# Kernel optimization log

Hardware: AMD Instinct MI355X
Metric: run time of the kernel (lower is better)

Reference implementation:

```python
import jax, jax.numpy as jnp
import numpy as np

N_ITER = 50


def sparsemax_bisect(X, n_iter=N_ITER):
    # entmax-style bisection for sparsemax (alpha=2): p = clip(X - tau, 0), sum(p) = 1
    d = X.shape[-1]
    max_val = jnp.max(X, axis=-1, keepdims=True)          # [N, 1]
    tau_lo = max_val - 1.0                                # f(tau_lo) >= 0
    tau_hi = max_val - 1.0 / d                            # f(tau_hi) <= 0
    f_lo = jnp.sum(jnp.clip(X - tau_lo, 0.0), axis=-1, keepdims=True) - 1.0
    dm0 = tau_hi - tau_lo

    def body(_, carry):
        tau_lo, dm, _tau_m = carry
        dm = dm * 0.5
        tau_m = tau_lo + dm
        f_m = jnp.sum(jnp.clip(X - tau_m, 0.0), axis=-1, keepdims=True) - 1.0
        tau_lo = jnp.where(f_m * f_lo >= 0, tau_m, tau_lo)
        return (tau_lo, dm, tau_m)

    _, _, tau_m = jax.lax.fori_loop(0, n_iter, body, (tau_lo, dm0, tau_lo))
    # p from the final midpoint, exactly as in entmax's sparsemax_bisect
    return jnp.clip(X - tau_m, 0.0)


def setup_inputs() -> dict:
    key = jax.random.key(0)
    X = jax.random.normal(key, (4096, 32000), dtype=jnp.float32)
    return {"X": X}


def reference(X):
    p_star = sparsemax_bisect(X, N_ITER)
    p_star = p_star / jnp.sum(p_star, axis=-1, keepdims=True)
    # log(0) -> -inf, matching torch.log on exact zeros
    sup = p_star > 0
    return jnp.where(sup, jnp.log(jnp.where(sup, p_star, 1.0)), -jnp.inf)
```

## Files before the change

kernel.cpp:

```cpp
#include <hip/hip_runtime.h>
#include <math.h>


typedef float f32x4 __attribute__((ext_vector_type(4)));

#define ROWS 4096
#define COLS 32000
#define NV4  (COLS / 4)
#define TPB  256
#define WPB  (TPB / 64)
#define U    4
#define SEG  512
#define CAP  (SEG * WPB)
#define REGC 4
#define SENT (-1e38f)
#define QMIN (1e-37f)

__global__ __launch_bounds__(TPB, 6)
void logsparsemax_v8_kernel(const float* __restrict__ X,
                            float* __restrict__ Y) {
    __shared__ float s_cand[CAP];
    __shared__ int   s_cidx[CAP];
    __shared__ float s_wmax[WPB];
    __shared__ int   s_wcnt[WPB];
    __shared__ float s_res[2];

    const int tid  = threadIdx.x;
    const int lane = tid & 63;
    const int wid  = tid >> 6;
    const int row  = blockIdx.x;
    const float* __restrict__ Xr = X + (size_t)row * COLS;
    const f32x4* __restrict__ X4 = (const f32x4*)Xr;
    float* __restrict__ Yr = Y + (size_t)row * COLS;
    f32x4* __restrict__ Y4 = (f32x4*)Yr;

    const f32x4 sent4 = {SENT, SENT, SENT, SENT};
    const int sbase = wid * SEG;

    float wmax = -INFINITY;
    float thr  = -INFINITY;
    int   cnt  = 0;

    int i = tid;
    f32x4 cur[U];
    #pragma unroll
    for (int u = 0; u < U; ++u) cur[u] = X4[i + u * TPB];

    while (i + (U - 1) * TPB < NV4) {
        const int inext = i + U * TPB;
        const bool hn = (inext + (U - 1) * TPB < NV4);
        f32x4 nxt[U];
        if (hn) {
            #pragma unroll
            for (int u = 0; u < U; ++u) nxt[u] = X4[inext + u * TPB];
        }
        #pragma unroll
        for (int u = 0; u < U; ++u) Y4[i + u * TPB] = sent4;

        float mall = -INFINITY;
        #pragma unroll
        for (int u = 0; u < U; ++u)
            mall = fmaxf(mall, fmaxf(fmaxf(cur[u].x, cur[u].y), fmaxf(cur[u].z, cur[u].w)));

        if (__ballot(mall > thr) != 0ull) {
            float t = mall;
            #pragma unroll
            for (int off = 32; off > 0; off >>= 1)
                t = fmaxf(t, __shfl_xor(t, off, 64));
            wmax = fmaxf(wmax, t);
            thr  = wmax - 1.0f;
            #pragma unroll
            for (int u = 0; u < U; ++u) {
                float vv[4] = {cur[u].x, cur[u].y, cur[u].z, cur[u].w};
                #pragma unroll
                for (int c = 0; c < 4; ++c) {
                    bool p = vv[c] > thr;
                    unsigned long long m = __ballot(p);
                    if (p) {
                        int pos = cnt + __popcll(m & ((1ull << lane) - 1ull));
                        if (pos < SEG) {
                            s_cand[sbase + pos] = vv[c];
                            s_cidx[sbase + pos] = 4 * (i + u * TPB) + c;
                        }
                    }
                    cnt += __popcll(m);
                }
            }
        }

        #pragma unroll
        for (int u = 0; u < U; ++u) cur[u] = nxt[u];
        i = inext;
    }
    for (; i < NV4; i += TPB) {
        f32x4 a = X4[i];
        Y4[i] = sent4;
        float mall = fmaxf(fmaxf(a.x, a.y), fmaxf(a.z, a.w));
        if (__ballot(mall > thr) != 0ull) {
            float t = mall;
            #pragma unroll
            for (int off = 32; off > 0; off >>= 1)
                t = fmaxf(t, __shfl_xor(t, off, 64));
            wmax = fmaxf(wmax, t);
            thr  = wmax - 1.0f;
            float vv[4] = {a.x, a.y, a.z, a.w};
            #pragma unroll
            for (int c = 0; c < 4; ++c) {
                bool p = vv[c] > thr;
                unsigned long long m = __ballot(p);
                if (p) {
                    int pos = cnt + __popcll(m & ((1ull << lane) - 1ull));
                    if (pos < SEG) {
                        s_cand[sbase + pos] = vv[c];
                        s_cidx[sbase + pos] = 4 * i + c;
                    }
                }
                cnt += __popcll(m);
            }
        }
    }

    if (lane == 0) { s_wmax[wid] = wmax; s_wcnt[wid] = cnt; }
    __syncthreads();

    const float bmax = fmaxf(fmaxf(s_wmax[0], s_wmax[1]), fmaxf(s_wmax[2], s_wmax[3]));
    const float tau_lo0 = bmax - 1.0f;
    const float tau_hi0 = bmax - (float)(1.0 / (double)COLS);
    const bool  fast = (s_wcnt[0] <= SEG) && (s_wcnt[1] <= SEG) &&
                       (s_wcnt[2] <= SEG) && (s_wcnt[3] <= SEG);

    if (wid == 0) {
        int nf = 0;
        if (fast) {
            for (int w = 0; w < WPB; ++w) {
                const int cw = s_wcnt[w];
                for (int j0 = 0; j0 < cw; j0 += 64) {
                    const int j = j0 + lane;
                    const bool in = (j < cw);
                    float v  = in ? s_cand[w * SEG + j] : 0.0f;
                    int   ix = in ? s_cidx[w * SEG + j] : 0;
                    bool  k  = in && (v > tau_lo0);
                    unsigned long long m = __ballot(k);
                    if (k) {
                        int pos = nf + __popcll(m & ((1ull << lane) - 1ull));
                        s_cand[pos] = v;
                        s_cidx[pos] = ix;
                    }
                    nf += __popcll(m);
                }
            }
        }

        float creg[REGC];
        #pragma unroll
        for (int k = 0; k < REGC; ++k) {
            int j = lane + 64 * k;
            creg[k] = (fast && j < nf) ? s_cand[j] : SENT;
        }

        auto fsum = [&](float tau) -> float {
            float acc = 0.0f;
            if (fast) {
                #pragma unroll
                for (int k = 0; k < REGC; ++k) acc += fmaxf(creg[k] - tau, 0.0f);
                for (int j = 64 * REGC + lane; j < nf; j += 64)
                    acc += fmaxf(s_cand[j] - tau, 0.0f);
            } else {
                for (int j = lane; j < COLS; j += 64)
                    acc += fmaxf(Xr[j] - tau, 0.0f);
            }
            #pragma unroll
            for (int off = 32; off > 0; off >>= 1)
                acc += __shfl_xor(acc, off, 64);
            return acc;
        };

        float tau_lo = tau_lo0;
        float dm     = tau_hi0 - tau_lo0;
        float tau_m  = tau_lo;
        const float f_lo = fsum(tau_lo) - 1.0f;
        for (int it = 0; it < 50; ++it) {
            dm *= 0.5f;
            float tcur = tau_lo + dm;
            tau_m = tcur;
            if (tcur == tau_lo) break;
            float f_m = fsum(tcur) - 1.0f;
            if (f_m * f_lo >= 0.0f) tau_lo = tcur;
        }
        const float ssum = fsum(tau_m);
        if (lane == 0) { s_res[0] = tau_m; s_res[1] = ssum; }

        if (fast) {
            const float lsm = logf(fmaxf(ssum, QMIN));
            for (int j = lane; j < nf; j += 64) {
                float r = s_cand[j] - tau_m;
                if (r > 0.0f)
                    Yr[s_cidx[j]] = logf(fmaxf(r, QMIN)) - lsm;
            }
        }
    }
    __syncthreads();

    if (!fast) {
        const float tau = s_res[0];
        const float lsm = logf(fmaxf(s_res[1], QMIN));
        for (int v4i = tid; v4i < NV4; v4i += TPB) {
            f32x4 v = X4[v4i];
            f32x4 o;
            float r;
            r = v.x - tau; o.x = (r > 0.0f) ? logf(fmaxf(r, QMIN)) - lsm : SENT;
            r = v.y - tau; o.y = (r > 0.0f) ? logf(fmaxf(r, QMIN)) - lsm : SENT;
            r = v.z - tau; o.z = (r > 0.0f) ? logf(fmaxf(r, QMIN)) - lsm : SENT;
            r = v.w - tau; o.w = (r > 0.0f) ? logf(fmaxf(r, QMIN)) - lsm : SENT;
            Y4[v4i] = o;
        }
    }
}

extern "C" void kernel_launch(void* const* d_in, const int* in_sizes, int n_in,
                              void* d_out, int out_size, void* d_ws, size_t ws_size,
                              hipStream_t stream) {
    const float* X = (const float*)d_in[0];
    float* Y = (float*)d_out;
    logsparsemax_v8_kernel<<<dim3(ROWS), dim3(TPB), 0, stream>>>(X, Y);
}
```

Baseline: 221.7 us.

## Use fixed threshold with per-thread register candidate lists in streaming pass

Replaces the dynamic running-max threshold and per-element wave ballots in the streaming loop with a fixed constant threshold (2.5) and per-thread register lists of up to 12 candidates. These are compacted into shared memory once after the pass. If the row max minus one falls below the constant, or any list overflows, a fallback rescans the row from global memory. The aim is to drop the wave-wide shuffles and ballots from the bandwidth-bound hot loop. The cost is more register pressure and a tuning that relies on the input distribution (normal data with large row maxima).

```diff
diff --git a/kernel.cpp b/kernel.cpp
--- a/kernel.cpp
+++ b/kernel.cpp
@@ -10,6 +10,8 @@
 #define TPB  256
 #define WPB  (TPB / 64)
 #define U    4
+#define THR  2.5f
+#define LCAP 12
 #define SEG  512
 #define CAP  (SEG * WPB)
 #define REGC 4
@@ -17,8 +19,8 @@
 #define QMIN (1e-37f)
 
 __global__ __launch_bounds__(TPB, 6)
-void logsparsemax_v8_kernel(const float* __restrict__ X,
-                            float* __restrict__ Y) {
+void logsparsemax_v16_kernel(const float* __restrict__ X,
+                             float* __restrict__ Y) {
     __shared__ float s_cand[CAP];
     __shared__ int   s_cidx[CAP];
     __shared__ float s_wmax[WPB];
@@ -37,9 +39,37 @@
     const f32x4 sent4 = {SENT, SENT, SENT, SENT};
     const int sbase = wid * SEG;
 
-    float wmax = -INFINITY;
-    float thr  = -INFINITY;
-    int   cnt  = 0;
+    float rm0 = -INFINITY, rm1 = -INFINITY, rm2 = -INFINITY, rm3 = -INFINITY;
+    float cv0, cv1, cv2, cv3, cv4, cv5, cv6, cv7, cv8, cv9, cv10, cv11;
+    int   ci0, ci1, ci2, ci3, ci4, ci5, ci6, ci7, ci8, ci9, ci10, ci11;
+    int   cnt = 0;
+
+    #define INSERT(val, idx)  do {                                    \
+        if      (cnt == 0)  { cv0  = (val); ci0  = (idx); }           \
+        else if (cnt == 1)  { cv1  = (val); ci1  = (idx); }           \
+        else if (cnt == 2)  { cv2  = (val); ci2  = (idx); }           \
+        else if (cnt == 3)  { cv3  = (val); ci3  = (idx); }           \
+        else if (cnt == 4)  { cv4  = (val); ci4  = (idx); }           \
+        else if (cnt == 5)  { cv5  = (val); ci5  = (idx); }           \
+        else if (cnt == 6)  { cv6  = (val); ci6  = (idx); }           \
+        else if (cnt == 7)  { cv7  = (val); ci7  = (idx); }           \
+        else if (cnt == 8)  { cv8  = (val); ci8  = (idx); }           \
+        else if (cnt == 9)  { cv9  = (val); ci9  = (idx); }           \
+        else if (cnt == 10) { cv10 = (val); ci10 = (idx); }           \
+        else if (cnt == 11) { cv11 = (val); ci11 = (idx); }           \
+        cnt++;                                                        \
+    } while (0)
+
+    #define PROC(vec, vbase, rmv) do {                                          \
+        float _m = fmaxf(fmaxf((vec).x, (vec).y), fmaxf((vec).z, (vec).w));     \
+        rmv = fmaxf(rmv, _m);                                                   \
+        if (_m > THR) {                \
+            if ((vec).x > THR) INSERT((vec).x, 4*(vbase)+0);                    \
+            if ((vec).y > THR) INSERT((vec).y, 4*(vbase)+1);                    \
+            if ((vec).z > THR) INSERT((vec).z, 4*(vbase)+2);                    \
+            if ((vec).w > THR) INSERT((vec).w, 4*(vbase)+3);                    \
+        }                                                                       \
+    } while (0)
 
     int i = tid;
     f32x4 cur[U];
@@ -57,36 +87,10 @@
         #pragma unroll
         for (int u = 0; u < U; ++u) Y4[i + u * TPB] = sent4;
 
-        float mall = -INFINITY;
-        #pragma unroll
-        for (int u = 0; u < U; ++u)
-            mall = fmaxf(mall, fmaxf(fmaxf(cur[u].x, cur[u].y), fmaxf(cur[u].z, cur[u].w)));
-
-        if (__ballot(mall > thr) != 0ull) {
-            float t = mall;
-            #pragma unroll
-            for (int off = 32; off > 0; off >>= 1)
-                t = fmaxf(t, __shfl_xor(t, off, 64));
-            wmax = fmaxf(wmax, t);
-            thr  = wmax - 1.0f;
-            #pragma unroll
-            for (int u = 0; u < U; ++u) {
-                float vv[4] = {cur[u].x, cur[u].y, cur[u].z, cur[u].w};
-                #pragma unroll
-                for (int c = 0; c < 4; ++c) {
-                    bool p = vv[c] > thr;
-                    unsigned long long m = __ballot(p);
-                    if (p) {
-                        int pos = cnt + __popcll(m & ((1ull << lane) - 1ull));
-                        if (pos < SEG) {
-                            s_cand[sbase + pos] = vv[c];
-                            s_cidx[sbase + pos] = 4 * (i + u * TPB) + c;
-                        }
-                    }
-                    cnt += __popcll(m);
-                }
-            }
-        }
+        PROC(cur[0], i + 0 * TPB, rm0);
+        PROC(cur[1], i + 1 * TPB, rm1);
+        PROC(cur[2], i + 2 * TPB, rm2);
+        PROC(cur[3], i + 3 * TPB, rm3);
 
         #pragma unroll
         for (int u = 0; u < U; ++u) cur[u] = nxt[u];
@@ -95,43 +99,79 @@
     for (; i < NV4; i += TPB) {
         f32x4 a = X4[i];
         Y4[i] = sent4;
-        float mall = fmaxf(fmaxf(a.x, a.y), fmaxf(a.z, a.w));
-        if (__ballot(mall > thr) != 0ull) {
-            float t = mall;
-            #pragma unroll
-            for (int off = 32; off > 0; off >>= 1)
-                t = fmaxf(t, __shfl_xor(t, off, 64));
-            wmax = fmaxf(wmax, t);
-            thr  = wmax - 1.0f;
-            float vv[4] = {a.x, a.y, a.z, a.w};
-            #pragma unroll
-            for (int c = 0; c < 4; ++c) {
-                bool p = vv[c] > thr;
-                unsigned long long m = __ballot(p);
-                if (p) {
-                    int pos = cnt + __popcll(m & ((1ull << lane) - 1ull));
-                    if (pos < SEG) {
-                        s_cand[sbase + pos] = vv[c];
-                        s_cidx[sbase + pos] = 4 * i + c;
-                    }
-                }
-                cnt += __popcll(m);
-            }
-        }
-    }
-
-    if (lane == 0) { s_wmax[wid] = wmax; s_wcnt[wid] = cnt; }
+        PROC(a, i, rm0);
+    }
+    #undef PROC
+    #undef INSERT
+
+    float wm = fmaxf(fmaxf(rm0, rm1), fmaxf(rm2, rm3));
+    #pragma unroll
+    for (int off = 32; off > 0; off >>= 1)
+        wm = fmaxf(wm, __shfl_xor(wm, off, 64));
+
+    int wcnt = 0;
+    #define DUMP(k, cvk, cik) do {                                              \
+        bool has = (cnt > (k));                                                 \
+        unsigned long long m = __ballot(has);                                   \
+        if (has) {                                                              \
+            int pos = wcnt + __popcll(m & ((1ull << lane) - 1ull));             \
+            if (pos < SEG) { s_cand[sbase + pos] = (cvk); s_cidx[sbase + pos] = (cik); } \
+        }                                                                       \
+        wcnt += __popcll(m);                                                    \
+    } while (0)
+    DUMP(0, cv0, ci0);  DUMP(1, cv1, ci1);  DUMP(2, cv2, ci2);   DUMP(3, cv3, ci3);
+    DUMP(4, cv4, ci4);  DUMP(5, cv5, ci5);  DUMP(6, cv6, ci6);   DUMP(7, cv7, ci7);
+    DUMP(8, cv8, ci8);  DUMP(9, cv9, ci9);  DUMP(10, cv10, ci10); DUMP(11, cv11, ci11);
+    #undef DUMP
+
+    const unsigned long long ovf = __ballot(cnt > LCAP);
+    if (lane == 0) {
+        s_wmax[wid] = wm;
+        s_wcnt[wid] = (ovf != 0ull || wcnt > SEG) ? -1 : wcnt;
+    }
     __syncthreads();
 
     const float bmax = fmaxf(fmaxf(s_wmax[0], s_wmax[1]), fmaxf(s_wmax[2], s_wmax[3]));
     const float tau_lo0 = bmax - 1.0f;
     const float tau_hi0 = bmax - (float)(1.0 / (double)COLS);
-    const bool  fast = (s_wcnt[0] <= SEG) && (s_wcnt[1] <= SEG) &&
-                       (s_wcnt[2] <= SEG) && (s_wcnt[3] <= SEG);
+
+    bool segs_ok = (tau_lo0 >= THR);
+    #pragma unroll
+    for (int w = 0; w < WPB; ++w) segs_ok = segs_ok && (s_wcnt[w] >= 0);
+
+    if (!segs_ok) {
+        int cnt2 = 0;
+        const int q0 = wid * (NV4 / WPB);
+        const int q1 = q0 + (NV4 / WPB);
+        for (int j = q0 + lane; j < q1; j += 64) {
+            f32x4 v = X4[j];
+            float vv[4] = {v.x, v.y, v.z, v.w};
+            #pragma unroll
+            for (int c = 0; c < 4; ++c) {
+                bool p = vv[c] > tau_lo0;
+                unsigned long long m = __ballot(p);
+                if (p) {
+                    int pos = cnt2 + __popcll(m & ((1ull << lane) - 1ull));
+                    if (pos < SEG) {
+                        s_cand[sbase + pos] = vv[c];
+                        s_cidx[sbase + pos] = 4 * j + c;
+                    }
+                }
+                cnt2 += __popcll(m);
+            }
+        }
+        if (lane == 0) s_wcnt[wid] = cnt2;
+        __syncthreads();
+    }
+
+    const bool fastv = (s_wcnt[0] >= 0 && s_wcnt[0] <= SEG) &&
+                       (s_wcnt[1] >= 0 && s_wcnt[1] <= SEG) &&
+                       (s_wcnt[2] >= 0 && s_wcnt[2] <= SEG) &&
+                       (s_wcnt[3] >= 0 && s_wcnt[3] <= SEG);
 
     if (wid == 0) {
         int nf = 0;
-        if (fast) {
+        if (fastv) {
             for (int w = 0; w < WPB; ++w) {
                 const int cw = s_wcnt[w];
                 for (int j0 = 0; j0 < cw; j0 += 64) {
@@ -155,12 +195,12 @@
         #pragma unroll
         for (int k = 0; k < REGC; ++k) {
             int j = lane + 64 * k;
-            creg[k] = (fast && j < nf) ? s_cand[j] : SENT;
+            creg[k] = (fastv && j < nf) ? s_cand[j] : SENT;
         }
 
         auto fsum = [&](float tau) -> float {
             float acc = 0.0f;
-            if (fast) {
+            if (fastv) {
                 #pragma unroll
                 for (int k = 0; k < REGC; ++k) acc += fmaxf(creg[k] - tau, 0.0f);
                 for (int j = 64 * REGC + lane; j < nf; j += 64)
@@ -190,7 +230,7 @@
         const float ssum = fsum(tau_m);
         if (lane == 0) { s_res[0] = tau_m; s_res[1] = ssum; }
 
-        if (fast) {
+        if (fastv) {
             const float lsm = logf(fmaxf(ssum, QMIN));
             for (int j = lane; j < nf; j += 64) {
                 float r = s_cand[j] - tau_m;
@@ -201,7 +241,7 @@
     }
     __syncthreads();
 
-    if (!fast) {
+    if (!fastv) {
         const float tau = s_res[0];
         const float lsm = logf(fmaxf(s_res[1], QMIN));
         for (int v4i = tid; v4i < NV4; v4i += TPB) {
@@ -222,5 +262,5 @@
                               hipStream_t stream) {
     const float* X = (const float*)d_in[0];
     float* Y = (float*)d_out;
-    logsparsemax_v8_kernel<<<dim3(ROWS), dim3(TPB), 0, stream>>>(X, Y);
+    logsparsemax_v16_kernel<<<dim3(ROWS), dim3(TPB), 0, stream>>>(X, Y);
 }
```

Result: slower. 230.9 us (+4.2%).
